# Optimization experiments

Measured on AMD Instinct MI355X. Metric: run time of the kernel, lower is better.

The kernel has to match this reference:

```python
import math
import jax, jax.numpy as jnp
import numpy as np

H = 12
D = 64  # head dim

def _heads(x):
    # [b, n, h*d] -> [b, h, n, d]
    b, n, _ = x.shape
    return x.reshape(b, n, H, D).transpose(0, 2, 1, 3)

def setup_inputs() -> dict:
    key = jax.random.key(0)
    ks = jax.random.split(key, 9)
    hs = 768
    s = 1.0 / math.sqrt(hs)
    return {
        "query_states": jax.random.normal(ks[0], (8, 1024, hs), jnp.float32),
        "key_states": jax.random.normal(ks[1], (8, 1024, hs), jnp.float32),
        "Wd": jax.random.normal(ks[2], (hs, hs), jnp.float32) * s,
        "Wq": jax.random.normal(ks[3], (hs, hs), jnp.float32) * s,
        "bq": jax.random.normal(ks[4], (hs,), jnp.float32) * 0.01,
        "Wk": jax.random.normal(ks[5], (hs, hs), jnp.float32) * s,
        "bk": jax.random.normal(ks[6], (hs,), jnp.float32) * 0.01,
        "Wv": jax.random.normal(ks[7], (hs, hs), jnp.float32) * s,
        "bv": jax.random.normal(ks[8], (hs,), jnp.float32) * 0.01,
    }

def reference(query_states, key_states, Wd, Wq, bq, Wk, bk, Wv, bv):
    # projections (torch Linear: x @ W.T + b)
    qd = _heads(query_states @ Wd.T)          # [b,h,n,d]
    kd = _heads(key_states @ Wd.T)
    q = _heads(query_states @ Wq.T + bq)
    k = _heads(key_states @ Wk.T + bk)
    v = _heads(key_states @ Wv.T + bv)
    # -0.5 * cdist(qd, kd)^2 = -0.5*(|qd|^2 + |kd|^2) + qd@kd^T
    qd_sq = jnp.sum(qd * qd, axis=-1)          # [b,h,n]
    kd_sq = jnp.sum(kd * kd, axis=-1)          # [b,h,m]
    quad = (qd @ jnp.swapaxes(kd, -1, -2)
            - 0.5 * qd_sq[..., :, None]
            - 0.5 * kd_sq[..., None, :])       # [b,h,n,m]
    lin = q @ jnp.swapaxes(k, -1, -2)          # [b,h,n,m]
    scores = (quad + lin) / math.sqrt(D)
    probs = jax.nn.softmax(scores, axis=-1)
    ctx = probs @ v                            # [b,h,n,d]
    b, _, n, _ = ctx.shape
    return ctx.transpose(0, 2, 1, 3).reshape(b, n, H * D)
```

## Files before the change

kernel.cpp:

```cpp
#include <hip/hip_runtime.h>
#include <stdint.h>

typedef __attribute__((ext_vector_type(8))) short short8;
typedef __attribute__((ext_vector_type(4))) short short4v;
typedef __attribute__((ext_vector_type(4))) float f32x4;
typedef __attribute__((ext_vector_type(16))) float f32x16;
typedef __attribute__((ext_vector_type(4))) int int4v;

static __device__ __forceinline__ unsigned short f2b(float f) {
  unsigned int u = __builtin_bit_cast(unsigned int, f);
  u += 0x7fffu + ((u >> 16) & 1u);
  return (unsigned short)(u >> 16);
}
static __device__ __forceinline__ float b2f(unsigned short b) {
  unsigned int u = ((unsigned int)b) << 16;
  return __builtin_bit_cast(float, u);
}

#define GLD16(gp, lp)                                                          \
  __builtin_amdgcn_global_load_lds(                                            \
      (const __attribute__((address_space(1))) void*)(gp),                     \
      (__attribute__((address_space(3))) void*)(lp), 16, 0, 0)

#define MFMA16 __builtin_amdgcn_mfma_f32_16x16x32_bf16
#define MFMA32 __builtin_amdgcn_mfma_f32_32x32x16_bf16

#define CVTPK(dst, lo, hi)                                                     \
  asm("v_cvt_pk_bf16_f32 %0, %1, %2" : "=v"(dst) : "v"(lo), "v"(hi))
#define PLSWAP(x, y)                                                           \
  asm volatile("v_permlane32_swap_b32 %0, %1" : "+v"(x), "+v"(y))

#define QSC 0.18033688011112113f
#define C2 0.09016844005556057f

__global__ void cvt_kernel(const float* __restrict__ q,
                           const float* __restrict__ k,
                           const float* __restrict__ Wd,
                           const float* __restrict__ Wq,
                           const float* __restrict__ Wk,
                           const float* __restrict__ Wv,
                           unsigned short* __restrict__ Xq,
                           unsigned short* __restrict__ Xk,
                           unsigned short* __restrict__ Wcq,
                           unsigned short* __restrict__ Wck) {
  const int bx = blockIdx.x;
  const float* src;
  unsigned short* dst;
  int i;
  if (bx < 12288) {
    const bool lo = bx < 6144;
    src = lo ? q : k;
    dst = lo ? Xq : Xk;
    i = (lo ? bx : bx - 6144) * 256 + threadIdx.x;
  } else {
    const int wb = bx - 12288;
    const int seg = wb / 576;
    i = (wb - seg * 576) * 256 + threadIdx.x;
    switch (seg) {
      case 0: src = Wd; dst = Wcq; break;
      case 1: src = Wq; dst = Wcq + 589824; break;
      case 2: src = Wd; dst = Wck; break;
      case 3: src = Wk; dst = Wck + 589824; break;
      default: src = Wv; dst = Wck + 1179648; break;
    }
  }
  float4 v = reinterpret_cast<const float4*>(src)[i];
  short4v o;
  o.x = (short)f2b(v.x);
  o.y = (short)f2b(v.y);
  o.z = (short)f2b(v.z);
  o.w = (short)f2b(v.w);
  reinterpret_cast<short4v*>(dst)[i] = o;
}

__global__ __launch_bounds__(512, 4) void proj_kernel(
    const unsigned short* __restrict__ Xq, const unsigned short* __restrict__ Xk,
    const unsigned short* __restrict__ Wcq, const unsigned short* __restrict__ Wck,
    const float* __restrict__ bq, const float* __restrict__ bk,
    const float* __restrict__ bv, unsigned short* __restrict__ Qc,
    unsigned short* __restrict__ Kc, unsigned short* __restrict__ Vt) {
  __shared__ __align__(16) short lds[2][384 * 32];
  const int by = blockIdx.y;
  const bool mode0 = (by < 6);
  const unsigned short* X = mode0 ? Xq : Xk;
  const unsigned short* W = mode0 ? Wcq : Wck;
  const int col0 = (mode0 ? by : by - 6) * 256;
  const int row0 = blockIdx.x * 128;
  const int tid = threadIdx.x;
  const int lane = tid & 63;
  const int wid = tid >> 6;
  const int wm = wid >> 2;
  const int wn = wid & 3;
  const int l15 = lane & 15, l4 = lane >> 4;
  const int RSWZ = (l4 ^ ((l15 >> 1) & 3)) << 4;

  f32x4 acc[4][4];
#pragma unroll
  for (int i = 0; i < 4; ++i)
#pragma unroll
    for (int j = 0; j < 4; ++j) acc[i][j] = (f32x4){0.f, 0.f, 0.f, 0.f};

  auto stage = [&](int bufi, int k0) {
    {
      const int c = tid;
      const int r = c >> 2;
      const int sl = (c & 3) ^ ((c >> 3) & 3);
      const unsigned short* gp = X + (size_t)(row0 + r) * 768 + k0 + sl * 8;
      GLD16(gp, (char*)&lds[bufi][0] + (size_t)c * 16);
    }
#pragma unroll
    for (int iss = 0; iss < 2; ++iss) {
      const int c = iss * 512 + tid;
      const int r = c >> 2;
      const int sl = (c & 3) ^ ((c >> 3) & 3);
      const unsigned short* gp = W + (size_t)(col0 + r) * 768 + k0 + sl * 8;
      GLD16(gp, (char*)&lds[bufi][0] + 8192 + (size_t)c * 16);
    }
  };

  stage(0, 0);
  asm volatile("s_waitcnt vmcnt(0)" ::: "memory");
  __builtin_amdgcn_s_barrier();

  for (int kt = 0; kt < 24; ++kt) {
    const int cb = kt & 1;
    if (kt < 23) stage(cb ^ 1, (kt + 1) * 32);

    const char* Ab = (const char*)&lds[cb][0];
    const char* Bb = (const char*)&lds[cb][0] + 8192;
    short8 a[4], b[4];
#pragma unroll
    for (int mt = 0; mt < 4; ++mt) {
      const int r = wm * 64 + mt * 16 + l15;
      a[mt] = *reinterpret_cast<const short8*>(Ab + r * 64 + RSWZ);
    }
#pragma unroll
    for (int nt = 0; nt < 4; ++nt) {
      const int r = wn * 64 + nt * 16 + l15;
      b[nt] = *reinterpret_cast<const short8*>(Bb + r * 64 + RSWZ);
    }
    __builtin_amdgcn_s_setprio(1);
#pragma unroll
    for (int mt = 0; mt < 4; ++mt)
#pragma unroll
      for (int nt = 0; nt < 4; ++nt)
        acc[mt][nt] = MFMA16(a[mt], b[nt], acc[mt][nt], 0, 0, 0);
    __builtin_amdgcn_s_setprio(0);
    asm volatile("s_waitcnt vmcnt(0) lgkmcnt(0)" ::: "memory");
    __builtin_amdgcn_s_barrier();
  }

  const int mat = mode0 ? (col0 >= 768 ? 1 : 0) : ((by - 6) / 3);
  const int cbase = col0 - mat * 768 + wn * 64;
  const float* barr = mode0 ? bq : (mat == 2 ? bv : bk);
  if (!mode0 && mat == 2) {
#pragma unroll
    for (int nt = 0; nt < 4; ++nt) {
      const int cc = cbase + nt * 16 + l15;
      const int hh = cc >> 6, dd = cc & 63;
      const float bias = barr[cc];
#pragma unroll
      for (int mt = 0; mt < 4; ++mt) {
        const int row = row0 + wm * 64 + mt * 16 + l4 * 4;
        const int bb = row >> 10, nn = row & 1023;
        short4v pv;
#pragma unroll
        for (int i = 0; i < 4; ++i)
          pv[i] = (short)f2b(acc[mt][nt][i] + bias);
        *reinterpret_cast<short4v*>(
            Vt + ((size_t)(bb * 12 + hh) * 64 + dd) * 1024 + nn) = pv;
      }
    }
  } else {
    const float scale = mode0 ? QSC : 1.0f;
    unsigned short* outC = mode0 ? Qc : Kc;
#pragma unroll
    for (int nt = 0; nt < 4; ++nt) {
      const int cc = cbase + nt * 16 + l15;
      const int hh = cc >> 6, dd = cc & 63;
      const float bias = (mat >= 1) ? barr[cc] : 0.f;
#pragma unroll
      for (int mt = 0; mt < 4; ++mt) {
#pragma unroll
        for (int i = 0; i < 4; ++i) {
          const int row = row0 + wm * 64 + mt * 16 + l4 * 4 + i;
          const int bb = row >> 10, nn = row & 1023;
          outC[((size_t)(bb * 12 + hh) * 1024 + nn) * 128 + mat * 64 + dd] =
              f2b((acc[mt][nt][i] + bias) * scale);
        }
      }
    }
  }
}

__global__ __launch_bounds__(256) void wv_kernel(
    const unsigned short* __restrict__ Kc, unsigned short* __restrict__ wq,
    const unsigned short* __restrict__ Vt, unsigned short* __restrict__ Vs) {
  __shared__ float wf[1024];
  const int bh = blockIdx.x;
  const int t = threadIdx.x;
  const int part = t & 3;
  const unsigned short* Kb = Kc + (size_t)bh * 1024 * 128;
#pragma unroll
  for (int it = 0; it < 16; ++it) {
    const int key = it * 64 + (t >> 2);
    const short8* p =
        reinterpret_cast<const short8*>(Kb + (size_t)key * 128 + part * 16);
    float s = 0.f;
    short8 x0 = p[0], x1 = p[1];
#pragma unroll
    for (int j = 0; j < 8; ++j) {
      const float f0 = b2f((unsigned short)x0[j]);
      const float f1 = b2f((unsigned short)x1[j]);
      s += f0 * f0 + f1 * f1;
    }
    s += __shfl_xor(s, 1);
    s += __shfl_xor(s, 2);
    if (part == 0) {
      const unsigned short wb = f2b(__builtin_amdgcn_exp2f(-s * C2));
      wf[key] = b2f(wb);
      wq[(size_t)bh * 1024 + key] = wb;
    }
  }
  __syncthreads();
  const unsigned short* Vb = Vt + (size_t)bh * 64 * 1024;
  unsigned short* Ob = Vs + (size_t)bh * 64 * 1024;
#pragma unroll
  for (int i = 0; i < 32; ++i) {
    const int e0 = (i * 256 + t) * 8;
    const int k0 = e0 & 1023;
    short8 v = *reinterpret_cast<const short8*>(Vb + e0);
#pragma unroll
    for (int j = 0; j < 8; ++j)
      v[j] = (short)f2b(b2f((unsigned short)v[j]) * wf[k0 + j]);
    *reinterpret_cast<short8*>(Ob + e0) = v;
  }
}

__global__ __launch_bounds__(256, 3) void attn_kernel(
    const unsigned short* __restrict__ Qc, const unsigned short* __restrict__ Kc,
    const unsigned short* __restrict__ Vs, const unsigned short* __restrict__ wq,
    float* __restrict__ out) {
  __shared__ __align__(16) short kbuf[2][64 * 128];
  __shared__ __align__(16) short vbuf[2][64 * 64];
  __shared__ __align__(16) short wbuf[1024];

  const int bh = blockIdx.x % 96;
  const int qb = blockIdx.x / 96;
  const int b = bh / 12, h = bh - b * 12;
  const int lane = threadIdx.x & 63;
  const int w = threadIdx.x >> 6;
  const int l31 = lane & 31, l5 = lane >> 5;

  const unsigned short* Kg = Kc + (size_t)bh * 1024 * 128;
  const unsigned short* Vg = Vs + (size_t)bh * 64 * 1024;

  auto stageK = [&](int bufi, int kb) {
#pragma unroll
    for (int i = 0; i < 4; ++i) {
      const int slot = i * 256 + threadIdx.x;
      const int row = slot >> 4;
      const int d0 = ((slot & 15) ^ (row & 15)) * 8;
      const unsigned short* gp = Kg + (size_t)(kb * 64 + row) * 128 + d0;
      GLD16(gp, (char*)(&kbuf[bufi][0]) + (i * 256 + w * 64) * 16);
    }
  };
  auto stageV = [&](int bufi, int kb) {
#pragma unroll
    for (int i = 0; i < 2; ++i) {
      const int slot = i * 256 + threadIdx.x;
      const int row = slot >> 3;
      const int k0 = ((slot & 7) ^ (row & 7)) * 8;
      const unsigned short* gp = Vg + (size_t)row * 1024 + kb * 64 + k0;
      GLD16(gp, (char*)(&vbuf[bufi][0]) + (i * 256 + w * 64) * 16);
    }
  };

  stageK(0, 0);
  stageV(0, 0);
  if (w < 2) {
    const unsigned short* gp = wq + (size_t)bh * 1024 + (w * 64 + lane) * 8;
    GLD16(gp, (char*)(&wbuf[0]) + w * 1024);
  }

  const unsigned short* Qb =
      Qc + ((size_t)bh * 1024 + qb * 128 + w * 32 + l31) * 128 + l5 * 8;
  short8 qf[8];
#pragma unroll
  for (int s = 0; s < 8; ++s)
    qf[s] = *reinterpret_cast<const short8*>(Qb + s * 16);

  f32x16 o0, o1, la;
#pragma unroll
  for (int r = 0; r < 16; ++r) {
    o0[r] = 0.f;
    o1[r] = 0.f;
    la[r] = 0.f;
  }
  float m = -1e30f;

  const int S4 = (lane & 15) << 4;
  const int S3 = (lane & 7) << 4;
  const int ko = l5 * 16;

  asm volatile("s_waitcnt vmcnt(0)" ::: "memory");
  __syncthreads();

  int buf = 0;
  for (int kb = 0; kb < 16; ++kb) {
    if (kb < 15) {
      stageK(buf ^ 1, kb + 1);
      stageV(buf ^ 1, kb + 1);
    }

    const char* kB = (const char*)(&kbuf[buf][0]) + l31 * 256;
    f32x16 s0, s1;
#pragma unroll
    for (int r = 0; r < 16; ++r) {
      s0[r] = 0.f;
      s1[r] = 0.f;
    }
    __builtin_amdgcn_s_setprio(1);
#pragma unroll
    for (int s = 0; s < 8; ++s) {
      const int off = (s * 32 + ko) ^ S4;
      short8 a0 = *reinterpret_cast<const short8*>(kB + off);
      short8 a1 = *reinterpret_cast<const short8*>(kB + 8192 + off);
      s0 = MFMA32(a0, qf[s], s0, 0, 0, 0);
      s1 = MFMA32(a1, qf[s], s1, 0, 0, 0);
    }
    __builtin_amdgcn_s_setprio(0);

    float mx = s0[0];
#pragma unroll
    for (int r = 1; r < 16; ++r) mx = fmaxf(mx, s0[r]);
#pragma unroll
    for (int r = 0; r < 16; ++r) mx = fmaxf(mx, s1[r]);
    mx = fmaxf(mx, __shfl_xor(mx, 32));

    if (!__all(mx <= m + 11.0f)) {
      const float mn = fmaxf(m, mx);
      const float c = __builtin_amdgcn_exp2f(m - mn);
      m = mn;
      float cr[16];
#pragma unroll
      for (int r = 0; r < 16; ++r)
        cr[r] = __shfl(c, (r & 3) + 8 * (r >> 2) + 4 * l5);
#pragma unroll
      for (int r = 0; r < 16; ++r) {
        la[r] *= cr[r];
        o0[r] *= cr[r];
        o1[r] *= cr[r];
      }
    }

#pragma unroll
    for (int r = 0; r < 16; ++r) {
      s0[r] = __builtin_amdgcn_exp2f(s0[r] - m);
      s1[r] = __builtin_amdgcn_exp2f(s1[r] - m);
    }
    unsigned int u[16];
#pragma unroll
    for (int j = 0; j < 8; ++j) {
      CVTPK(u[j], s0[2 * j], s0[2 * j + 1]);
      CVTPK(u[8 + j], s1[2 * j], s1[2 * j + 1]);
    }
    PLSWAP(u[0], u[2]);
    PLSWAP(u[1], u[3]);
    PLSWAP(u[4], u[6]);
    PLSWAP(u[5], u[7]);
    PLSWAP(u[8], u[10]);
    PLSWAP(u[9], u[11]);
    PLSWAP(u[12], u[14]);
    PLSWAP(u[13], u[15]);
    short8 pa[4];
    {
      int4v t0 = {(int)u[0], (int)u[1], (int)u[2], (int)u[3]};
      int4v t1 = {(int)u[4], (int)u[5], (int)u[6], (int)u[7]};
      int4v t2 = {(int)u[8], (int)u[9], (int)u[10], (int)u[11]};
      int4v t3 = {(int)u[12], (int)u[13], (int)u[14], (int)u[15]};
      pa[0] = __builtin_bit_cast(short8, t0);
      pa[1] = __builtin_bit_cast(short8, t1);
      pa[2] = __builtin_bit_cast(short8, t2);
      pa[3] = __builtin_bit_cast(short8, t3);
    }

    const char* vB = (const char*)(&vbuf[buf][0]) + l31 * 128;
    const char* wB = (const char*)(&wbuf[0]) + kb * 128 + ko;
    __builtin_amdgcn_s_setprio(1);
#pragma unroll
    for (int kk = 0; kk < 4; ++kk) {
      const int off = (kk * 32 + ko) ^ S3;
      short8 v0 = *reinterpret_cast<const short8*>(vB + off);
      short8 v1 = *reinterpret_cast<const short8*>(vB + 4096 + off);
      short8 wf = *reinterpret_cast<const short8*>(wB + kk * 32);
      o0 = MFMA32(pa[kk], v0, o0, 0, 0, 0);
      o1 = MFMA32(pa[kk], v1, o1, 0, 0, 0);
      la = MFMA32(pa[kk], wf, la, 0, 0, 0);
    }
    __builtin_amdgcn_s_setprio(0);

    asm volatile("s_waitcnt vmcnt(0)" ::: "memory");
    __syncthreads();
    buf ^= 1;
  }

  const int qbase = b * 1024 + qb * 128 + w * 32;
#pragma unroll
  for (int r = 0; r < 16; ++r) {
    const float iv = __builtin_amdgcn_rcpf(la[r]);
    const int q = qbase + (r & 3) + 8 * (r >> 2) + 4 * l5;
    float* op = out + (size_t)q * 768 + h * 64 + l31;
    op[0] = o0[r] * iv;
    op[32] = o1[r] * iv;
  }
}

extern "C" void kernel_launch(void* const* d_in, const int* in_sizes, int n_in,
                              void* d_out, int out_size, void* d_ws,
                              size_t ws_size, hipStream_t stream) {
  const float* query = (const float*)d_in[0];
  const float* key = (const float*)d_in[1];
  const float* Wd = (const float*)d_in[2];
  const float* Wq = (const float*)d_in[3];
  const float* bq = (const float*)d_in[4];
  const float* Wk = (const float*)d_in[5];
  const float* bk = (const float*)d_in[6];
  const float* Wv = (const float*)d_in[7];
  const float* bv = (const float*)d_in[8];
  float* out = (float*)d_out;

  char* p = (char*)d_ws;
  auto alloc = [&](size_t n) {
    char* r = p;
    p += (n + 255) & ~(size_t)255;
    return r;
  };
  unsigned short* Xq = (unsigned short*)alloc(8192ULL * 768 * 2);
  unsigned short* Xk = (unsigned short*)alloc(8192ULL * 768 * 2);
  unsigned short* Wcq = (unsigned short*)alloc(1536ULL * 768 * 2);
  unsigned short* Wck = (unsigned short*)alloc(2304ULL * 768 * 2);
  unsigned short* Qc = (unsigned short*)alloc(96ULL * 1024 * 128 * 2);
  unsigned short* Kc = (unsigned short*)alloc(96ULL * 1024 * 128 * 2);
  unsigned short* Vt = (unsigned short*)alloc(96ULL * 64 * 1024 * 2);
  unsigned short* wqv = (unsigned short*)alloc(96ULL * 1024 * 2);
  unsigned short* Vs = Xk;

  cvt_kernel<<<15168, 256, 0, stream>>>(query, key, Wd, Wq, Wk, Wv, Xq, Xk,
                                        Wcq, Wck);

  proj_kernel<<<dim3(64, 15), 512, 0, stream>>>(Xq, Xk, Wcq, Wck, bq, bk, bv,
                                                Qc, Kc, Vt);

  wv_kernel<<<96, 256, 0, stream>>>(Kc, wqv, Vt, Vs);

  attn_kernel<<<768, 256, 0, stream>>>(Qc, Kc, Vs, wqv, out);
}
```

Measured before the change: 156.8 us.

## Fuse activation conversion and key-weight computation into projection and attention kernels

```diff
diff --git a/kernel.cpp b/kernel.cpp
--- a/kernel.cpp
+++ b/kernel.cpp
@@ -33,36 +33,23 @@
 #define QSC 0.18033688011112113f
 #define C2 0.09016844005556057f
 
-__global__ void cvt_kernel(const float* __restrict__ q,
-                           const float* __restrict__ k,
-                           const float* __restrict__ Wd,
-                           const float* __restrict__ Wq,
-                           const float* __restrict__ Wk,
-                           const float* __restrict__ Wv,
-                           unsigned short* __restrict__ Xq,
-                           unsigned short* __restrict__ Xk,
-                           unsigned short* __restrict__ Wcq,
-                           unsigned short* __restrict__ Wck) {
+__global__ void cvtw_kernel(const float* __restrict__ Wd,
+                            const float* __restrict__ Wq,
+                            const float* __restrict__ Wk,
+                            const float* __restrict__ Wv,
+                            unsigned short* __restrict__ Wcq,
+                            unsigned short* __restrict__ Wck) {
   const int bx = blockIdx.x;
+  const int seg = bx / 576;
+  const int i = (bx - seg * 576) * 256 + threadIdx.x;
   const float* src;
   unsigned short* dst;
-  int i;
-  if (bx < 12288) {
-    const bool lo = bx < 6144;
-    src = lo ? q : k;
-    dst = lo ? Xq : Xk;
-    i = (lo ? bx : bx - 6144) * 256 + threadIdx.x;
-  } else {
-    const int wb = bx - 12288;
-    const int seg = wb / 576;
-    i = (wb - seg * 576) * 256 + threadIdx.x;
-    switch (seg) {
-      case 0: src = Wd; dst = Wcq; break;
-      case 1: src = Wq; dst = Wcq + 589824; break;
-      case 2: src = Wd; dst = Wck; break;
-      case 3: src = Wk; dst = Wck + 589824; break;
-      default: src = Wv; dst = Wck + 1179648; break;
-    }
+  switch (seg) {
+    case 0: src = Wd; dst = Wcq; break;
+    case 1: src = Wq; dst = Wcq + 589824; break;
+    case 2: src = Wd; dst = Wck; break;
+    case 3: src = Wk; dst = Wck + 589824; break;
+    default: src = Wv; dst = Wck + 1179648; break;
   }
   float4 v = reinterpret_cast<const float4*>(src)[i];
   short4v o;
@@ -74,15 +61,16 @@
 }
 
 __global__ __launch_bounds__(512, 4) void proj_kernel(
-    const unsigned short* __restrict__ Xq, const unsigned short* __restrict__ Xk,
+    const float* __restrict__ Xqf, const float* __restrict__ Xkf,
     const unsigned short* __restrict__ Wcq, const unsigned short* __restrict__ Wck,
     const float* __restrict__ bq, const float* __restrict__ bk,
     const float* __restrict__ bv, unsigned short* __restrict__ Qc,
-    unsigned short* __restrict__ Kc, unsigned short* __restrict__ Vt) {
+    unsigned short* __restrict__ Kc, unsigned short* __restrict__ Vt,
+    float* __restrict__ wqf) {
   __shared__ __align__(16) short lds[2][384 * 32];
   const int by = blockIdx.y;
   const bool mode0 = (by < 6);
-  const unsigned short* X = mode0 ? Xq : Xk;
+  const float* Xf = mode0 ? Xqf : Xkf;
   const unsigned short* W = mode0 ? Wcq : Wck;
   const int col0 = (mode0 ? by : by - 6) * 256;
   const int row0 = blockIdx.x * 128;
@@ -100,14 +88,24 @@
 #pragma unroll
     for (int j = 0; j < 4; ++j) acc[i][j] = (f32x4){0.f, 0.f, 0.f, 0.f};
 
-  auto stage = [&](int bufi, int k0) {
-    {
-      const int c = tid;
-      const int r = c >> 2;
-      const int sl = (c & 3) ^ ((c >> 3) & 3);
-      const unsigned short* gp = X + (size_t)(row0 + r) * 768 + k0 + sl * 8;
-      GLD16(gp, (char*)&lds[bufi][0] + (size_t)c * 16);
-    }
+  const int Ar = tid >> 2;
+  const int Asl = (tid & 3) ^ ((tid >> 3) & 3);
+  const float* Agp = Xf + (size_t)(row0 + Ar) * 768 + Asl * 8;
+
+  auto loadA = [&](int k0, float4& a0, float4& a1) {
+    a0 = *reinterpret_cast<const float4*>(Agp + k0);
+    a1 = *reinterpret_cast<const float4*>(Agp + k0 + 4);
+  };
+  auto writeA = [&](int bufi, const float4& a0, const float4& a1) {
+    unsigned int u0, u1, u2, u3;
+    CVTPK(u0, a0.x, a0.y);
+    CVTPK(u1, a0.z, a0.w);
+    CVTPK(u2, a1.x, a1.y);
+    CVTPK(u3, a1.z, a1.w);
+    int4v v = {(int)u0, (int)u1, (int)u2, (int)u3};
+    *reinterpret_cast<int4v*>((char*)&lds[bufi][0] + (size_t)tid * 16) = v;
+  };
+  auto stageB = [&](int bufi, int k0) {
 #pragma unroll
     for (int iss = 0; iss < 2; ++iss) {
       const int c = iss * 512 + tid;
@@ -118,13 +116,22 @@
     }
   };
 
-  stage(0, 0);
-  asm volatile("s_waitcnt vmcnt(0)" ::: "memory");
+  {
+    float4 a0, a1;
+    loadA(0, a0, a1);
+    stageB(0, 0);
+    writeA(0, a0, a1);
+  }
+  asm volatile("s_waitcnt vmcnt(0) lgkmcnt(0)" ::: "memory");
   __builtin_amdgcn_s_barrier();
 
   for (int kt = 0; kt < 24; ++kt) {
     const int cb = kt & 1;
-    if (kt < 23) stage(cb ^ 1, (kt + 1) * 32);
+    float4 xa0, xa1;
+    if (kt < 23) {
+      loadA((kt + 1) * 32, xa0, xa1);
+      stageB(cb ^ 1, (kt + 1) * 32);
+    }
 
     const char* Ab = (const char*)&lds[cb][0];
     const char* Bb = (const char*)&lds[cb][0] + 8192;
@@ -146,11 +153,35 @@
       for (int nt = 0; nt < 4; ++nt)
         acc[mt][nt] = MFMA16(a[mt], b[nt], acc[mt][nt], 0, 0, 0);
     __builtin_amdgcn_s_setprio(0);
+    if (kt < 23) writeA(cb ^ 1, xa0, xa1);
     asm volatile("s_waitcnt vmcnt(0) lgkmcnt(0)" ::: "memory");
     __builtin_amdgcn_s_barrier();
   }
 
   const int mat = mode0 ? (col0 >= 768 ? 1 : 0) : ((by - 6) / 3);
+
+  if (!mode0 && mat == 0) {
+    const int hh = ((by - 6) << 2) + wn;
+#pragma unroll
+    for (int mt = 0; mt < 4; ++mt) {
+#pragma unroll
+      for (int i = 0; i < 4; ++i) {
+        float s = acc[mt][0][i] * acc[mt][0][i] + acc[mt][1][i] * acc[mt][1][i] +
+                  acc[mt][2][i] * acc[mt][2][i] + acc[mt][3][i] * acc[mt][3][i];
+        s += __shfl_xor(s, 1);
+        s += __shfl_xor(s, 2);
+        s += __shfl_xor(s, 4);
+        s += __shfl_xor(s, 8);
+        if (l15 == 0) {
+          const int row = row0 + wm * 64 + mt * 16 + l4 * 4 + i;
+          const int bb = row >> 10, nn = row & 1023;
+          wqf[(size_t)(bb * 12 + hh) * 1024 + nn] =
+              __builtin_amdgcn_exp2f(-s * C2);
+        }
+      }
+    }
+  }
+
   const int cbase = col0 - mat * 768 + wn * 64;
   const float* barr = mode0 ? bq : (mat == 2 ? bv : bk);
   if (!mode0 && mat == 2) {
@@ -193,57 +224,13 @@
   }
 }
 
-__global__ __launch_bounds__(256) void wv_kernel(
-    const unsigned short* __restrict__ Kc, unsigned short* __restrict__ wq,
-    const unsigned short* __restrict__ Vt, unsigned short* __restrict__ Vs) {
-  __shared__ float wf[1024];
-  const int bh = blockIdx.x;
-  const int t = threadIdx.x;
-  const int part = t & 3;
-  const unsigned short* Kb = Kc + (size_t)bh * 1024 * 128;
-#pragma unroll
-  for (int it = 0; it < 16; ++it) {
-    const int key = it * 64 + (t >> 2);
-    const short8* p =
-        reinterpret_cast<const short8*>(Kb + (size_t)key * 128 + part * 16);
-    float s = 0.f;
-    short8 x0 = p[0], x1 = p[1];
-#pragma unroll
-    for (int j = 0; j < 8; ++j) {
-      const float f0 = b2f((unsigned short)x0[j]);
-      const float f1 = b2f((unsigned short)x1[j]);
-      s += f0 * f0 + f1 * f1;
-    }
-    s += __shfl_xor(s, 1);
-    s += __shfl_xor(s, 2);
-    if (part == 0) {
-      const unsigned short wb = f2b(__builtin_amdgcn_exp2f(-s * C2));
-      wf[key] = b2f(wb);
-      wq[(size_t)bh * 1024 + key] = wb;
-    }
-  }
-  __syncthreads();
-  const unsigned short* Vb = Vt + (size_t)bh * 64 * 1024;
-  unsigned short* Ob = Vs + (size_t)bh * 64 * 1024;
-#pragma unroll
-  for (int i = 0; i < 32; ++i) {
-    const int e0 = (i * 256 + t) * 8;
-    const int k0 = e0 & 1023;
-    short8 v = *reinterpret_cast<const short8*>(Vb + e0);
-#pragma unroll
-    for (int j = 0; j < 8; ++j)
-      v[j] = (short)f2b(b2f((unsigned short)v[j]) * wf[k0 + j]);
-    *reinterpret_cast<short8*>(Ob + e0) = v;
-  }
-}
-
 __global__ __launch_bounds__(256, 3) void attn_kernel(
     const unsigned short* __restrict__ Qc, const unsigned short* __restrict__ Kc,
-    const unsigned short* __restrict__ Vs, const unsigned short* __restrict__ wq,
+    const unsigned short* __restrict__ Vt, const float* __restrict__ wqf,
     float* __restrict__ out) {
   __shared__ __align__(16) short kbuf[2][64 * 128];
   __shared__ __align__(16) short vbuf[2][64 * 64];
-  __shared__ __align__(16) short wbuf[1024];
+  __shared__ __align__(16) float wfb[1024];
 
   const int bh = blockIdx.x % 96;
   const int qb = blockIdx.x / 96;
@@ -253,7 +240,7 @@
   const int l31 = lane & 31, l5 = lane >> 5;
 
   const unsigned short* Kg = Kc + (size_t)bh * 1024 * 128;
-  const unsigned short* Vg = Vs + (size_t)bh * 64 * 1024;
+  const unsigned short* Vg = Vt + (size_t)bh * 64 * 1024;
 
   auto stageK = [&](int bufi, int kb) {
 #pragma unroll
@@ -278,9 +265,9 @@
 
   stageK(0, 0);
   stageV(0, 0);
-  if (w < 2) {
-    const unsigned short* gp = wq + (size_t)bh * 1024 + (w * 64 + lane) * 8;
-    GLD16(gp, (char*)(&wbuf[0]) + w * 1024);
+  {
+    const float* gp = wqf + (size_t)bh * 1024 + threadIdx.x * 4;
+    GLD16(gp, (char*)(&wfb[0]) + w * 1024);
   }
 
   const unsigned short* Qb =
@@ -289,6 +276,10 @@
 #pragma unroll
   for (int s = 0; s < 8; ++s)
     qf[s] = *reinterpret_cast<const short8*>(Qb + s * 16);
+
+  short8 ones;
+#pragma unroll
+  for (int j = 0; j < 8; ++j) ones[j] = (short)0x3F80;
 
   f32x16 o0, o1, la;
 #pragma unroll
@@ -331,6 +322,14 @@
     }
     __builtin_amdgcn_s_setprio(0);
 
+    f32x4 w0v[4], w1v[4];
+#pragma unroll
+    for (int j = 0; j < 4; ++j) {
+      w0v[j] = *reinterpret_cast<const f32x4*>(&wfb[kb * 64 + j * 8 + 4 * l5]);
+      w1v[j] =
+          *reinterpret_cast<const f32x4*>(&wfb[kb * 64 + 32 + j * 8 + 4 * l5]);
+    }
+
     float mx = s0[0];
 #pragma unroll
     for (int r = 1; r < 16; ++r) mx = fmaxf(mx, s0[r]);
@@ -356,8 +355,8 @@
 
 #pragma unroll
     for (int r = 0; r < 16; ++r) {
-      s0[r] = __builtin_amdgcn_exp2f(s0[r] - m);
-      s1[r] = __builtin_amdgcn_exp2f(s1[r] - m);
+      s0[r] = __builtin_amdgcn_exp2f(s0[r] - m) * w0v[r >> 2][r & 3];
+      s1[r] = __builtin_amdgcn_exp2f(s1[r] - m) * w1v[r >> 2][r & 3];
     }
     unsigned int u[16];
 #pragma unroll
@@ -386,17 +385,15 @@
     }
 
     const char* vB = (const char*)(&vbuf[buf][0]) + l31 * 128;
-    const char* wB = (const char*)(&wbuf[0]) + kb * 128 + ko;
     __builtin_amdgcn_s_setprio(1);
 #pragma unroll
     for (int kk = 0; kk < 4; ++kk) {
       const int off = (kk * 32 + ko) ^ S3;
       short8 v0 = *reinterpret_cast<const short8*>(vB + off);
       short8 v1 = *reinterpret_cast<const short8*>(vB + 4096 + off);
-      short8 wf = *reinterpret_cast<const short8*>(wB + kk * 32);
       o0 = MFMA32(pa[kk], v0, o0, 0, 0, 0);
       o1 = MFMA32(pa[kk], v1, o1, 0, 0, 0);
-      la = MFMA32(pa[kk], wf, la, 0, 0, 0);
+      la = MFMA32(pa[kk], ones, la, 0, 0, 0);
     }
     __builtin_amdgcn_s_setprio(0);
 
@@ -436,23 +433,17 @@
     p += (n + 255) & ~(size_t)255;
     return r;
   };
-  unsigned short* Xq = (unsigned short*)alloc(8192ULL * 768 * 2);
-  unsigned short* Xk = (unsigned short*)alloc(8192ULL * 768 * 2);
   unsigned short* Wcq = (unsigned short*)alloc(1536ULL * 768 * 2);
   unsigned short* Wck = (unsigned short*)alloc(2304ULL * 768 * 2);
   unsigned short* Qc = (unsigned short*)alloc(96ULL * 1024 * 128 * 2);
   unsigned short* Kc = (unsigned short*)alloc(96ULL * 1024 * 128 * 2);
   unsigned short* Vt = (unsigned short*)alloc(96ULL * 64 * 1024 * 2);
-  unsigned short* wqv = (unsigned short*)alloc(96ULL * 1024 * 2);
-  unsigned short* Vs = Xk;
-
-  cvt_kernel<<<15168, 256, 0, stream>>>(query, key, Wd, Wq, Wk, Wv, Xq, Xk,
-                                        Wcq, Wck);
-
-  proj_kernel<<<dim3(64, 15), 512, 0, stream>>>(Xq, Xk, Wcq, Wck, bq, bk, bv,
-                                                Qc, Kc, Vt);
-
-  wv_kernel<<<96, 256, 0, stream>>>(Kc, wqv, Vt, Vs);
-
-  attn_kernel<<<768, 256, 0, stream>>>(Qc, Kc, Vs, wqv, out);
-}
+  float* wqf = (float*)alloc(96ULL * 1024 * 4);
+
+  cvtw_kernel<<<2880, 256, 0, stream>>>(Wd, Wq, Wk, Wv, Wcq, Wck);
+
+  proj_kernel<<<dim3(64, 15), 512, 0, stream>>>(query, key, Wcq, Wck, bq, bk,
+                                                bv, Qc, Kc, Vt, wqf);
+
+  attn_kernel<<<768, 256, 0, stream>>>(Qc, Kc, Vt, wqf, out);
+}
```

After: 140.3 us (median of 2 runs). 1.12x faster.
